# Optimization experiments

Measured on AMD Instinct MI355X. Metric: run time of the kernel, lower is better.

Reference implementation:

```python
import jax, jax.numpy as jnp
import numpy as np

NUM_HEADS = 32
HEAD_DIM = 128
HIDDEN = NUM_HEADS * HEAD_DIM
BLOCK = 128
ROPE_THETA = 10000.0
NEG_INF = -1e9


def _fp4_e2m1(x):
    # Simulated float_quantize(x, exp=2, man=1): E2M1 grid {0, .5, 1, 1.5, 2, 3, 4, 6},
    # round-to-nearest-even, saturate at +-6.
    a = jnp.abs(x)
    e = jnp.clip(jnp.floor(jnp.log2(jnp.maximum(a, 1e-30))), 0.0, 2.0)
    step = jnp.exp2(e) * 0.5  # mantissa LSB at this exponent
    q = jnp.clip(jnp.round(a / step) * step, 0.0, 6.0)
    return jnp.sign(x) * q


def quantize_mxfp4(v, block=BLOCK):
    # along_rows=False path: block over the sequence axis (after transpose(-1,-2)).
    b, h, s, d = v.shape
    t = jnp.swapaxes(v, -1, -2)  # [b,h,d,s]
    pad = (-s) % block
    t = jnp.pad(t, ((0, 0), (0, 0), (0, 0), (0, pad)))
    t = t.reshape(-1, block)
    amax = jnp.max(jnp.abs(t), axis=-1, keepdims=True)
    scale = jnp.exp2(jnp.ceil(jnp.log2(jnp.maximum(amax, 1e-30))) - 3.0)
    scale = jnp.where(amax == 0, 1.0, scale)
    t = _fp4_e2m1(t / scale) * scale
    t = t.reshape(b, h, d, s + pad)[..., :s]
    return jnp.swapaxes(t, -1, -2)


def _rotary(position_ids, dtype):
    # cos/sin: [b, s, head_dim]
    inv_freq = 1.0 / (ROPE_THETA ** (jnp.arange(0, HEAD_DIM, 2, dtype=jnp.float32) / HEAD_DIM))
    freqs = position_ids.astype(jnp.float32)[..., None] * inv_freq  # [b,s,d/2]
    emb = jnp.concatenate([freqs, freqs], axis=-1)
    return jnp.cos(emb).astype(dtype), jnp.sin(emb).astype(dtype)


def _rotate_half(x):
    x1, x2 = jnp.split(x, 2, axis=-1)
    return jnp.concatenate([-x2, x1], axis=-1)


def setup_inputs() -> dict:
    key = jax.random.key(0)
    ks = jax.random.split(key, 5)
    wscale = 1.0 / np.sqrt(HIDDEN)
    return {
        "hidden_states": jax.random.normal(ks[0], (2, 2048, HIDDEN), dtype=jnp.float32),
        "position_ids": jnp.arange(2048, dtype=jnp.int32)[None, :],
        "Wq": jax.random.normal(ks[1], (HIDDEN, HIDDEN), dtype=jnp.float32) * wscale,
        "Wk": jax.random.normal(ks[2], (HIDDEN, HIDDEN), dtype=jnp.float32) * wscale,
        "Wv": jax.random.normal(ks[3], (HIDDEN, HIDDEN), dtype=jnp.float32) * wscale,
        "Wo": jax.random.normal(ks[4], (HIDDEN, HIDDEN), dtype=jnp.float32) * wscale,
    }


def reference(hidden_states, position_ids, Wq, Wk, Wv, Wo):
    b, s, _ = hidden_states.shape

    # per-head channel ordering from ||row of v_proj||_2 (descending)
    norm3 = jnp.linalg.norm(Wv.astype(jnp.float32), ord=2, axis=-1)  # [HIDDEN]
    order = jnp.argsort(-norm3.reshape(NUM_HEADS, HEAD_DIM), axis=-1)  # [H, D]
    inverse_order = jnp.argsort(order, axis=-1)

    def proj(W):
        y = jnp.einsum('bsh,oh->bso', hidden_states, W)
        return y.reshape(b, s, NUM_HEADS, HEAD_DIM).transpose(0, 2, 1, 3)  # [b,H,s,D]

    q = proj(Wq)
    k = proj(Wk)
    v = proj(Wv)

    # reorder channels, mxfp4-quantize V along sequence blocks, restore order
    v = jnp.take_along_axis(v, order[None, :, None, :], axis=-1)
    v = quantize_mxfp4(v, BLOCK)
    v = jnp.take_along_axis(v, inverse_order[None, :, None, :], axis=-1)

    cos, sin = _rotary(position_ids, hidden_states.dtype)
    cos = cos[:, None, :, :]  # unsqueeze_dim=1
    sin = sin[:, None, :, :]
    q = q * cos + _rotate_half(q) * sin
    k = k * cos + _rotate_half(k) * sin

    scores = jnp.einsum('bhqd,bhkd->bhqk', q, k) / np.sqrt(HEAD_DIM)
    causal = jnp.tril(jnp.ones((s, s), dtype=bool))
    scores = jnp.where(causal[None, None], scores, NEG_INF)
    attn = jax.nn.softmax(scores.astype(jnp.float32), axis=-1).astype(q.dtype)

    out = jnp.einsum('bhqk,bhkd->bhqd', attn, v)
    out = out.transpose(0, 2, 1, 3).reshape(b, s, HIDDEN)
    return jnp.einsum('bso,ho->bsh', out, Wo)
```

## Files before the change

### kernel.cpp

```cpp
#include <hip/hip_runtime.h>
#include <math.h>

typedef unsigned short u16;
typedef unsigned int u32;
typedef short bf16x8 __attribute__((ext_vector_type(8)));
typedef float f32x4 __attribute__((ext_vector_type(4)));

#define MFMA16(a, b, c) __builtin_amdgcn_mfma_f32_16x16x32_bf16(a, b, c, 0, 0, 0)

static __device__ __forceinline__ u16 f2b(float f) {
  u32 u = __builtin_bit_cast(u32, f);
  u = (u + 0x7fffu + ((u >> 16) & 1u)) >> 16;
  return (u16)u;
}
static __device__ __forceinline__ float b2f(u16 h) {
  return __builtin_bit_cast(float, ((u32)h) << 16);
}
static __device__ __forceinline__ void gload16(const void* g, void* l) {
  __builtin_amdgcn_global_load_lds((const __attribute__((address_space(1))) void*)g,
                                   (__attribute__((address_space(3))) void*)l, 16, 0, 0);
}
static __device__ __forceinline__ void split2(float x, u16& hi, u16& lo) {
  hi = f2b(x);
  lo = f2b(x - b2f(hi));
}
static __device__ __forceinline__ float quant1(float x, float scale, float rs) {
  float y = fabsf(x) * rs;
  float st = y < 2.f ? 0.5f : (y < 4.f ? 1.f : 2.f);
  float iv = y < 2.f ? 2.f : (y < 4.f ? 1.f : 0.5f);
  float q = fminf(rintf(y * iv) * st, 6.f);
  return copysignf(q * scale, x);
}

__global__ __launch_bounds__(256) void k_cvt(const float* __restrict__ in, u16* __restrict__ out) {
  int i = blockIdx.x * 256 + threadIdx.x;
  float4 v = ((const float4*)in)[i];
  u32 lo = (u32)f2b(v.x) | ((u32)f2b(v.y) << 16);
  u32 hi = (u32)f2b(v.z) | ((u32)f2b(v.w) << 16);
  ((uint2*)out)[i] = make_uint2(lo, hi);
}

__global__ __launch_bounds__(256) void k_splt(const float* __restrict__ in,
                                              u16* __restrict__ hi, u16* __restrict__ lo) {
  int i = blockIdx.x * 256 + threadIdx.x;
  float4 v = ((const float4*)in)[i];
  u16 h[4], l[4];
  split2(v.x, h[0], l[0]);
  split2(v.y, h[1], l[1]);
  split2(v.z, h[2], l[2]);
  split2(v.w, h[3], l[3]);
  ((uint2*)hi)[i] = make_uint2((u32)h[0] | ((u32)h[1] << 16), (u32)h[2] | ((u32)h[3] << 16));
  ((uint2*)lo)[i] = make_uint2((u32)l[0] | ((u32)l[1] << 16), (u32)l[2] | ((u32)l[3] << 16));
}

__global__ __launch_bounds__(256) void k_rope_tab(const int* __restrict__ pid,
                                                  float* __restrict__ ct,
                                                  float* __restrict__ st) {
  int t = blockIdx.x * 256 + threadIdx.x;
  int s = t >> 6, i = t & 63;
  float inv = powf(10000.f, -(float)i * (1.f / 64.f));
  float a = (float)pid[s] * inv;
  ct[t] = cosf(a);
  st[t] = sinf(a);
}

template <int EPI>
__global__ __launch_bounds__(512, 2) void k_gemm8(const u16* __restrict__ A,
                                                  const u16* __restrict__ B,
                                                  void* __restrict__ outp,
                                                  const float* __restrict__ cost,
                                                  const float* __restrict__ sint) {
  __shared__ u16 Ls[2][2][2][8192];
  const int tid = threadIdx.x;
  const int wid = tid >> 6, lane = tid & 63;
  const int l15 = lane & 15, lhi = lane >> 4;
  const int wm = wid >> 2, wn = wid & 3;
  const int hib = wn >> 1, sub = wn & 1;

  const int bid = blockIdx.x;
  const int bx = 2 * (bid & 7) + (bid >> 7);
  const int by = (bid >> 3) & 15;
  const int mbase = by * 256, nbase = bx * 256;

  f32x4 acc[8][4];
#pragma unroll
  for (int mi = 0; mi < 8; ++mi)
#pragma unroll
    for (int nj = 0; nj < 4; ++nj) acc[mi][nj] = (f32x4){0.f, 0.f, 0.f, 0.f};

  auto stA = [&](int buf, int half, int ktile) {
    u16* dst = Ls[buf][0][half];
    const int k0 = ktile * 64;
#pragma unroll
    for (int i = 0; i < 2; ++i) {
      int idx = i * 512 + tid;
      int row = idx >> 3;
      int col = k0 + ((((idx & 7) << 4) ^ ((row & 7) << 4)) >> 1);
      gload16(A + (size_t)(mbase + half * 128 + row) * 4096 + col, (char*)dst + idx * 16);
    }
  };
  auto stB = [&](int buf, int half, int ktile) {
    u16* dst = Ls[buf][1][half];
    const int k0 = ktile * 64;
#pragma unroll
    for (int i = 0; i < 2; ++i) {
      int idx = i * 512 + tid;
      int row = idx >> 3;
      int col = k0 + ((((idx & 7) << 4) ^ ((row & 7) << 4)) >> 1);
      gload16(B + (size_t)(nbase + half * 128 + row) * 4096 + col, (char*)dst + idx * 16);
    }
  };

  stB(0, 0, 0);
  stB(0, 1, 0);
  stA(0, 0, 0);
  stA(0, 1, 0);
  stB(1, 0, 1);
  stB(1, 1, 1);

  const int NT = 64;
  for (int kt = 0; kt < NT; ++kt) {
    const int cur = kt & 1, nxt = cur ^ 1;
    const u16* Ab = Ls[cur][0][wm];
    const u16* Bb = Ls[cur][1][hib];
    bf16x8 aA[4][2], aB[4][2], bA[2][2], bB[2][2];

    if (kt + 1 < NT) stA(nxt, 0, kt + 1);
    if (kt == NT - 1) {
      asm volatile("s_waitcnt vmcnt(0)" ::: "memory");
    } else {
      asm volatile("s_waitcnt vmcnt(6)" ::: "memory");
    }
    __builtin_amdgcn_s_barrier();
#pragma unroll
    for (int mi = 0; mi < 4; ++mi)
#pragma unroll
      for (int ks = 0; ks < 2; ++ks) {
        int row = mi * 16 + l15;
        int kk2 = (ks * 32 + lhi * 8) * 2;
        aA[mi][ks] = *(const bf16x8*)((const char*)Ab + row * 128 + (kk2 ^ ((row & 7) << 4)));
      }
#pragma unroll
    for (int nj = 0; nj < 2; ++nj)
#pragma unroll
      for (int ks = 0; ks < 2; ++ks) {
        int row = sub * 32 + nj * 16 + l15;
        int kk2 = (ks * 32 + lhi * 8) * 2;
        bA[nj][ks] = *(const bf16x8*)((const char*)Bb + row * 128 + (kk2 ^ ((row & 7) << 4)));
      }
    __builtin_amdgcn_s_setprio(1);
#pragma unroll
    for (int mi = 0; mi < 4; ++mi)
#pragma unroll
      for (int nj = 0; nj < 2; ++nj)
#pragma unroll
        for (int ks = 0; ks < 2; ++ks) acc[mi][nj] = MFMA16(aA[mi][ks], bA[nj][ks], acc[mi][nj]);
    __builtin_amdgcn_s_setprio(0);
    __builtin_amdgcn_s_barrier();

#pragma unroll
    for (int nj = 0; nj < 2; ++nj)
#pragma unroll
      for (int ks = 0; ks < 2; ++ks) {
        int row = 64 + sub * 32 + nj * 16 + l15;
        int kk2 = (ks * 32 + lhi * 8) * 2;
        bB[nj][ks] = *(const bf16x8*)((const char*)Bb + row * 128 + (kk2 ^ ((row & 7) << 4)));
      }
    if (kt + 1 < NT) stA(nxt, 1, kt + 1);
    __builtin_amdgcn_s_barrier();
    __builtin_amdgcn_s_setprio(1);
#pragma unroll
    for (int mi = 0; mi < 4; ++mi)
#pragma unroll
      for (int nj = 0; nj < 2; ++nj)
#pragma unroll
        for (int ks = 0; ks < 2; ++ks)
          acc[mi][nj + 2] = MFMA16(aA[mi][ks], bB[nj][ks], acc[mi][nj + 2]);
    __builtin_amdgcn_s_setprio(0);
    __builtin_amdgcn_s_barrier();

#pragma unroll
    for (int mi = 0; mi < 4; ++mi)
#pragma unroll
      for (int ks = 0; ks < 2; ++ks) {
        int row = 64 + mi * 16 + l15;
        int kk2 = (ks * 32 + lhi * 8) * 2;
        aB[mi][ks] = *(const bf16x8*)((const char*)Ab + row * 128 + (kk2 ^ ((row & 7) << 4)));
      }
    if (kt + 2 < NT) stB(cur, 0, kt + 2);
    __builtin_amdgcn_s_barrier();
    __builtin_amdgcn_s_setprio(1);
#pragma unroll
    for (int mi = 0; mi < 4; ++mi)
#pragma unroll
      for (int nj = 0; nj < 2; ++nj)
#pragma unroll
        for (int ks = 0; ks < 2; ++ks)
          acc[mi + 4][nj] = MFMA16(aB[mi][ks], bA[nj][ks], acc[mi + 4][nj]);
    __builtin_amdgcn_s_setprio(0);
    __builtin_amdgcn_s_barrier();

    if (kt + 2 < NT) stB(cur, 1, kt + 2);
    __builtin_amdgcn_s_barrier();
    __builtin_amdgcn_s_setprio(1);
#pragma unroll
    for (int mi = 0; mi < 4; ++mi)
#pragma unroll
      for (int nj = 0; nj < 2; ++nj)
#pragma unroll
        for (int ks = 0; ks < 2; ++ks)
          acc[mi + 4][nj + 2] = MFMA16(aB[mi][ks], bB[nj][ks], acc[mi + 4][nj + 2]);
    __builtin_amdgcn_s_setprio(0);
    __builtin_amdgcn_s_barrier();
  }

  if constexpr (EPI == 3) {
    float* out = (float*)outp;
#pragma unroll
    for (int mi = 0; mi < 8; ++mi)
#pragma unroll
      for (int r = 0; r < 4; ++r) {
        size_t m = (size_t)(mbase + wm * 128 + mi * 16 + lhi * 4 + r);
#pragma unroll
        for (int nj = 0; nj < 4; ++nj) {
          int n = nbase + hib * 128 + (nj >> 1) * 64 + sub * 32 + (nj & 1) * 16 + l15;
          out[m * 4096 + n] = acc[mi][nj][r];
        }
      }
  } else {
    u16* qo = (u16*)outp;
    const int hgl = bx * 2 + hib;
#pragma unroll
    for (int mi = 0; mi < 8; ++mi)
#pragma unroll
      for (int r = 0; r < 4; ++r) {
        int m = mbase + wm * 128 + mi * 16 + lhi * 4 + r;
        int b = m >> 11, s = m & 2047;
        const float* ct = cost + (size_t)s * 64;
        const float* st = sint + (size_t)s * 64;
        size_t base = ((size_t)(b * 32 + hgl) * 2048 + s) * 128;
#pragma unroll
        for (int nj = 0; nj < 2; ++nj) {
          int d = sub * 32 + nj * 16 + l15;
          float c = ct[d], sn = st[d];
          float x1 = acc[mi][nj][r], x2 = acc[mi][nj + 2][r];
          qo[base + d] = f2b(x1 * c - x2 * sn);
          qo[base + d + 64] = f2b(x2 * c + x1 * sn);
        }
      }
  }
}

__global__ __launch_bounds__(512) void k_gemmv3(const u16* __restrict__ ahi,
                                                const u16* __restrict__ alo,
                                                const u16* __restrict__ bhi,
                                                const u16* __restrict__ blo,
                                                u16* __restrict__ vt) {
  __shared__ u16 Ls[2][4][8192];
  const int tid = threadIdx.x;
  const int wid = tid >> 6, lane = tid & 63;
  const int l15 = lane & 15, lhi = lane >> 4;
  const int wm = wid >> 2, wn = wid & 3;
  const int mbase = blockIdx.y * 128, nbase = blockIdx.x * 128;

  f32x4 acc[4][2];
#pragma unroll
  for (int mi = 0; mi < 4; ++mi)
#pragma unroll
    for (int nj = 0; nj < 2; ++nj) acc[mi][nj] = (f32x4){0.f, 0.f, 0.f, 0.f};

  auto stage = [&](int buf, int ktile) {
    const int k0 = ktile * 64;
#pragma unroll
    for (int i = 0; i < 2; ++i) {
      int idx = i * 512 + tid;
      int row = idx >> 3;
      int col = k0 + ((((idx & 7) << 4) ^ ((row & 7) << 4)) >> 1);
      size_t ga = (size_t)(mbase + row) * 4096 + col;
      size_t gb = (size_t)(nbase + row) * 4096 + col;
      gload16(ahi + ga, (char*)Ls[buf][0] + idx * 16);
      gload16(alo + ga, (char*)Ls[buf][1] + idx * 16);
      gload16(bhi + gb, (char*)Ls[buf][2] + idx * 16);
      gload16(blo + gb, (char*)Ls[buf][3] + idx * 16);
    }
  };

  stage(0, 0);

  const int NT = 64;
  for (int kt = 0; kt < NT; ++kt) {
    const int cur = kt & 1;
    if (kt < NT - 1) {
      stage(cur ^ 1, kt + 1);
      asm volatile("s_waitcnt vmcnt(8)" ::: "memory");
    } else {
      asm volatile("s_waitcnt vmcnt(0)" ::: "memory");
    }
    __builtin_amdgcn_s_barrier();

    bf16x8 ah[4][2], al[4][2], bh[2][2], bl[2][2];
#pragma unroll
    for (int mi = 0; mi < 4; ++mi)
#pragma unroll
      for (int ks = 0; ks < 2; ++ks) {
        int row = wm * 64 + mi * 16 + l15;
        int off = row * 128 + (((ks * 32 + lhi * 8) * 2) ^ ((row & 7) << 4));
        ah[mi][ks] = *(const bf16x8*)((const char*)Ls[cur][0] + off);
        al[mi][ks] = *(const bf16x8*)((const char*)Ls[cur][1] + off);
      }
#pragma unroll
    for (int nj = 0; nj < 2; ++nj)
#pragma unroll
      for (int ks = 0; ks < 2; ++ks) {
        int row = wn * 32 + nj * 16 + l15;
        int off = row * 128 + (((ks * 32 + lhi * 8) * 2) ^ ((row & 7) << 4));
        bh[nj][ks] = *(const bf16x8*)((const char*)Ls[cur][2] + off);
        bl[nj][ks] = *(const bf16x8*)((const char*)Ls[cur][3] + off);
      }
#pragma unroll
    for (int ks = 0; ks < 2; ++ks)
#pragma unroll
      for (int mi = 0; mi < 4; ++mi)
#pragma unroll
        for (int nj = 0; nj < 2; ++nj) {
          acc[mi][nj] = MFMA16(ah[mi][ks], bh[nj][ks], acc[mi][nj]);
          acc[mi][nj] = MFMA16(ah[mi][ks], bl[nj][ks], acc[mi][nj]);
          acc[mi][nj] = MFMA16(al[mi][ks], bh[nj][ks], acc[mi][nj]);
        }
    asm volatile("s_waitcnt lgkmcnt(0)" ::: "memory");
    __builtin_amdgcn_s_barrier();
  }

  const int h = nbase >> 7;
  float* red = (float*)Ls[0][0];
  float pam[2];
#pragma unroll
  for (int nj = 0; nj < 2; ++nj) {
    float a = 0.f;
#pragma unroll
    for (int mi = 0; mi < 4; ++mi)
#pragma unroll
      for (int r = 0; r < 4; ++r) a = fmaxf(a, fabsf(acc[mi][nj][r]));
    a = fmaxf(a, __shfl_xor(a, 16));
    a = fmaxf(a, __shfl_xor(a, 32));
    pam[nj] = a;
  }
  if (lhi == 0) {
#pragma unroll
    for (int nj = 0; nj < 2; ++nj) red[wid * 32 + nj * 16 + l15] = pam[nj];
  }
  __syncthreads();
#pragma unroll
  for (int nj = 0; nj < 2; ++nj) {
    int c = nj * 16 + l15;
    float amax = fmaxf(red[wn * 32 + c], red[(4 + wn) * 32 + c]);
    float scale = 1.f, rs = 1.f;
    if (amax > 0.f) {
      int e;
      float mant = frexpf(amax, &e);
      int cc = (mant == 0.5f) ? (e - 1) : e;
      scale = ldexpf(1.f, cc - 3);
      rs = ldexpf(1.f, 3 - cc);
    }
    int d = wn * 32 + c;
#pragma unroll
    for (int mi = 0; mi < 4; ++mi) {
      int m0 = mbase + wm * 64 + mi * 16 + lhi * 4;
      int b = m0 >> 11, s0 = m0 & 2047;
      uint2 pk;
      float v0 = quant1(acc[mi][nj][0], scale, rs);
      float v1 = quant1(acc[mi][nj][1], scale, rs);
      float v2 = quant1(acc[mi][nj][2], scale, rs);
      float v3 = quant1(acc[mi][nj][3], scale, rs);
      pk.x = (u32)f2b(v0) | ((u32)f2b(v1) << 16);
      pk.y = (u32)f2b(v2) | ((u32)f2b(v3) << 16);
      *(uint2*)(vt + ((size_t)(b * 32 + h) * 128 + d) * 2048 + s0) = pk;
    }
  }
}

template <int EPI>
__global__ __launch_bounds__(256) void k_gemm(const u16* __restrict__ A,
                                              const float* __restrict__ B,
                                              void* __restrict__ outp,
                                              const float* __restrict__ cost,
                                              const float* __restrict__ sint) {
  __shared__ u16 As[128 * 64];
  __shared__ u16 Bs[128 * 64];
  const int tid = threadIdx.x;
  const int w = tid >> 6, lane = tid & 63;
  const int l15 = lane & 15, lhi = lane >> 4;
  const int mbase = blockIdx.y * 128, nbase = blockIdx.x * 128;
  f32x4 acc[2][8];
#pragma unroll
  for (int i = 0; i < 2; ++i)
#pragma unroll
    for (int j = 0; j < 8; ++j) acc[i][j] = (f32x4){0.f, 0.f, 0.f, 0.f};

  const int brow = tid >> 1, bk = (tid & 1) * 32;
  const float* bsrc = B + (size_t)(nbase + brow) * 4096 + bk;

  for (int kt = 0; kt < 64; ++kt) {
    const int k0 = kt * 64;
#pragma unroll
    for (int i = 0; i < 4; ++i) {
      int idx = i * 256 + tid;
      int row = idx >> 3;
      int inb = ((idx & 7) << 4) ^ ((row & 7) << 4);
      gload16(A + (size_t)(mbase + row) * 4096 + (k0 + (inb >> 1)), (char*)As + idx * 16);
    }
    float4 bv[8];
    const float* bp = bsrc + k0;
#pragma unroll
    for (int c = 0; c < 8; ++c) bv[c] = *(const float4*)(bp + c * 4);
#pragma unroll
    for (int c = 0; c < 4; ++c) {
      uint4 pk;
      pk.x = (u32)f2b(bv[2 * c].x) | ((u32)f2b(bv[2 * c].y) << 16);
      pk.y = (u32)f2b(bv[2 * c].z) | ((u32)f2b(bv[2 * c].w) << 16);
      pk.z = (u32)f2b(bv[2 * c + 1].x) | ((u32)f2b(bv[2 * c + 1].y) << 16);
      pk.w = (u32)f2b(bv[2 * c + 1].z) | ((u32)f2b(bv[2 * c + 1].w) << 16);
      int byte = brow * 128 + (((bk + c * 8) * 2) ^ ((brow & 7) << 4));
      *(uint4*)((char*)Bs + byte) = pk;
    }
    __syncthreads();
#pragma unroll
    for (int ks = 0; ks < 2; ++ks) {
      const int kk2 = (ks * 32 + lhi * 8) * 2;
      bf16x8 af[2], bfr[8];
#pragma unroll
      for (int i = 0; i < 2; ++i) {
        int row = w * 32 + i * 16 + l15;
        af[i] = *(const bf16x8*)((const char*)As + row * 128 + (kk2 ^ ((row & 7) << 4)));
      }
#pragma unroll
      for (int j = 0; j < 8; ++j) {
        int row = j * 16 + l15;
        bfr[j] = *(const bf16x8*)((const char*)Bs + row * 128 + (kk2 ^ ((row & 7) << 4)));
      }
#pragma unroll
      for (int i = 0; i < 2; ++i)
#pragma unroll
        for (int j = 0; j < 8; ++j) acc[i][j] = MFMA16(af[i], bfr[j], acc[i][j]);
    }
    __syncthreads();
  }

  const int h = nbase >> 7;
  if constexpr (EPI == 3) {
    float* out = (float*)outp;
#pragma unroll
    for (int i = 0; i < 2; ++i)
#pragma unroll
      for (int r = 0; r < 4; ++r) {
        size_t m = (size_t)(mbase + w * 32 + i * 16 + lhi * 4 + r);
#pragma unroll
        for (int j = 0; j < 8; ++j) out[m * 4096 + nbase + j * 16 + l15] = acc[i][j][r];
      }
  } else {
    u16* qo = (u16*)outp;
#pragma unroll
    for (int i = 0; i < 2; ++i)
#pragma unroll
      for (int r = 0; r < 4; ++r) {
        int m = mbase + w * 32 + i * 16 + lhi * 4 + r;
        int b = m >> 11, s = m & 2047;
        const float* ct = cost + (size_t)s * 64;
        const float* st = sint + (size_t)s * 64;
        size_t base = ((size_t)(b * 32 + h) * 2048 + s) * 128;
#pragma unroll
        for (int j = 0; j < 4; ++j) {
          int d = j * 16 + l15;
          float c = ct[d], sn = st[d];
          float x1 = acc[i][j][r], x2 = acc[i][j + 4][r];
          qo[base + d] = f2b(x1 * c - x2 * sn);
          qo[base + d + 64] = f2b(x2 * c + x1 * sn);
        }
      }
  }
}

__global__ __launch_bounds__(256) void k_gemmv(const float* __restrict__ hsf,
                                               const float* __restrict__ Wv,
                                               u16* __restrict__ vt) {
  __shared__ u16 AsHi[128 * 64];
  __shared__ u16 AsLo[128 * 64];
  __shared__ u16 BsHi[128 * 64];
  __shared__ u16 BsLo[128 * 64];
  const int tid = threadIdx.x;
  const int w = tid >> 6, lane = tid & 63;
  const int l15 = lane & 15, lhi = lane >> 4;
  const int mbase = blockIdx.y * 128, nbase = blockIdx.x * 128;
  f32x4 acc[2][8];
#pragma unroll
  for (int i = 0; i < 2; ++i)
#pragma unroll
    for (int j = 0; j < 8; ++j) acc[i][j] = (f32x4){0.f, 0.f, 0.f, 0.f};

  const int srow = tid >> 1, sk = (tid & 1) * 32;
  const float* asrc = hsf + (size_t)(mbase + srow) * 4096 + sk;
  const float* bsrc = Wv + (size_t)(nbase + srow) * 4096 + sk;

  for (int kt = 0; kt < 64; ++kt) {
    const int k0 = kt * 64;
    float4 av[8], bv[8];
#pragma unroll
    for (int c = 0; c < 8; ++c) {
      av[c] = *(const float4*)(asrc + k0 + c * 4);
      bv[c] = *(const float4*)(bsrc + k0 + c * 4);
    }
#pragma unroll
    for (int c = 0; c < 4; ++c) {
      u16 h0, l0, h1, l1;
      float fa[8] = {av[2 * c].x, av[2 * c].y, av[2 * c].z, av[2 * c].w,
                     av[2 * c + 1].x, av[2 * c + 1].y, av[2 * c + 1].z, av[2 * c + 1].w};
      float fb[8] = {bv[2 * c].x, bv[2 * c].y, bv[2 * c].z, bv[2 * c].w,
                     bv[2 * c + 1].x, bv[2 * c + 1].y, bv[2 * c + 1].z, bv[2 * c + 1].w};
      u32 ph[4], pl[4], qh[4], ql[4];
#pragma unroll
      for (int t = 0; t < 4; ++t) {
        split2(fa[2 * t], h0, l0);
        split2(fa[2 * t + 1], h1, l1);
        ph[t] = (u32)h0 | ((u32)h1 << 16);
        pl[t] = (u32)l0 | ((u32)l1 << 16);
        split2(fb[2 * t], h0, l0);
        split2(fb[2 * t + 1], h1, l1);
        qh[t] = (u32)h0 | ((u32)h1 << 16);
        ql[t] = (u32)l0 | ((u32)l1 << 16);
      }
      int byte = srow * 128 + (((sk + c * 8) * 2) ^ ((srow & 7) << 4));
      *(uint4*)((char*)AsHi + byte) = make_uint4(ph[0], ph[1], ph[2], ph[3]);
      *(uint4*)((char*)AsLo + byte) = make_uint4(pl[0], pl[1], pl[2], pl[3]);
      *(uint4*)((char*)BsHi + byte) = make_uint4(qh[0], qh[1], qh[2], qh[3]);
      *(uint4*)((char*)BsLo + byte) = make_uint4(ql[0], ql[1], ql[2], ql[3]);
    }
    __syncthreads();
#pragma unroll
    for (int ks = 0; ks < 2; ++ks) {
      const int kk2 = (ks * 32 + lhi * 8) * 2;
      bf16x8 afh[2], afl[2];
#pragma unroll
      for (int i = 0; i < 2; ++i) {
        int row = w * 32 + i * 16 + l15;
        int off = row * 128 + (kk2 ^ ((row & 7) << 4));
        afh[i] = *(const bf16x8*)((const char*)AsHi + off);
        afl[i] = *(const bf16x8*)((const char*)AsLo + off);
      }
#pragma unroll
      for (int j = 0; j < 8; ++j) {
        int row = j * 16 + l15;
        int off = row * 128 + (kk2 ^ ((row & 7) << 4));
        bf16x8 bh = *(const bf16x8*)((const char*)BsHi + off);
        bf16x8 bl = *(const bf16x8*)((const char*)BsLo + off);
#pragma unroll
        for (int i = 0; i < 2; ++i) {
          acc[i][j] = MFMA16(afh[i], bh, acc[i][j]);
          acc[i][j] = MFMA16(afh[i], bl, acc[i][j]);
          acc[i][j] = MFMA16(afl[i], bh, acc[i][j]);
        }
      }
    }
    __syncthreads();
  }

  const int h = nbase >> 7;
  float pam[8];
#pragma unroll
  for (int j = 0; j < 8; ++j) {
    float a = 0.f;
#pragma unroll
    for (int i = 0; i < 2; ++i)
#pragma unroll
      for (int r = 0; r < 4; ++r) a = fmaxf(a, fabsf(acc[i][j][r]));
    a = fmaxf(a, __shfl_xor(a, 16));
    a = fmaxf(a, __shfl_xor(a, 32));
    pam[j] = a;
  }
  float* red = (float*)BsHi;
  if (lhi == 0) {
#pragma unroll
    for (int j = 0; j < 8; ++j) red[w * 128 + j * 16 + l15] = pam[j];
  }
  __syncthreads();
#pragma unroll
  for (int j = 0; j < 8; ++j) {
    float amax = fmaxf(fmaxf(red[0 * 128 + j * 16 + l15], red[1 * 128 + j * 16 + l15]),
                       fmaxf(red[2 * 128 + j * 16 + l15], red[3 * 128 + j * 16 + l15]));
    float scale = 1.f, rs = 1.f;
    if (amax > 0.f) {
      int e;
      float mant = frexpf(amax, &e);
      int c = (mant == 0.5f) ? (e - 1) : e;
      scale = ldexpf(1.f, c - 3);
      rs = ldexpf(1.f, 3 - c);
    }
#pragma unroll
    for (int i = 0; i < 2; ++i) {
      int m0 = mbase + w * 32 + i * 16 + lhi * 4;
      int b = m0 >> 11, s0 = m0 & 2047;
      int d = j * 16 + l15;
      uint2 pk;
      float v0 = quant1(acc[i][j][0], scale, rs);
      float v1 = quant1(acc[i][j][1], scale, rs);
      float v2 = quant1(acc[i][j][2], scale, rs);
      float v3 = quant1(acc[i][j][3], scale, rs);
      pk.x = (u32)f2b(v0) | ((u32)f2b(v1) << 16);
      pk.y = (u32)f2b(v2) | ((u32)f2b(v3) << 16);
      *(uint2*)(vt + ((size_t)(b * 32 + h) * 128 + d) * 2048 + s0) = pk;
    }
  }
}

__global__ __launch_bounds__(512) void k_attn(const u16* __restrict__ qg,
                                              const u16* __restrict__ kg,
                                              const u16* __restrict__ vtg,
                                              u16* __restrict__ ao) {
  __shared__ u16 Ks[2][64 * 128];
  __shared__ u16 Vs[2][128 * 64];
  __shared__ u16 Ps[8 * 16 * 72];
  const int qt = 15 - blockIdx.y;
  const int bh = blockIdx.x;
  const int tid = threadIdx.x, w = tid >> 6, lane = tid & 63;
  const int l15 = lane & 15, lhi = lane >> 4;
  const size_t bhoff = (size_t)bh * (2048 * 128);
  const float SC = 0.08838834764831845f;

  bf16x8 qf[4];
  {
    const int qrow = qt * 128 + w * 16 + l15;
    const u16* qp = qg + bhoff + (size_t)qrow * 128 + lhi * 8;
#pragma unroll
    for (int ks = 0; ks < 4; ++ks) qf[ks] = *(const bf16x8*)(qp + ks * 32);
  }
  f32x4 oacc[8];
#pragma unroll
  for (int dt = 0; dt < 8; ++dt) oacc[dt] = (f32x4){0.f, 0.f, 0.f, 0.f};
  float mrow[4] = {-1e30f, -1e30f, -1e30f, -1e30f};
  float lrow[4] = {0.f, 0.f, 0.f, 0.f};

  auto stage = [&](int buf, int kbase) {
#pragma unroll
    for (int i = 0; i < 2; ++i) {
      int idx = i * 512 + tid;
      int row = idx >> 4;
      int inb = ((idx & 15) << 4) ^ ((row & 15) << 4);
      gload16(kg + bhoff + (size_t)(kbase + row) * 128 + (inb >> 1), (char*)Ks[buf] + idx * 16);
    }
#pragma unroll
    for (int i = 0; i < 2; ++i) {
      int idx = i * 512 + tid;
      int row = idx >> 3;
      int inb = ((idx & 7) << 4) ^ ((row & 7) << 4);
      gload16(vtg + bhoff + (size_t)row * 2048 + kbase + (inb >> 1), (char*)Vs[buf] + idx * 16);
    }
  };

  const int nt = 2 * qt + 2;
  stage(0, 0);

  for (int kt = 0; kt < nt; ++kt) {
    const int cur = kt & 1;
    if (kt < nt - 1) {
      stage(cur ^ 1, (kt + 1) * 64);
      asm volatile("s_waitcnt vmcnt(4)" ::: "memory");
    } else {
      asm volatile("s_waitcnt vmcnt(0)" ::: "memory");
    }
    __builtin_amdgcn_s_barrier();

    f32x4 sc4[4];
#pragma unroll
    for (int j = 0; j < 4; ++j) sc4[j] = (f32x4){0.f, 0.f, 0.f, 0.f};
#pragma unroll
    for (int ks = 0; ks < 4; ++ks) {
      const int db = (ks * 32 + lhi * 8) * 2;
#pragma unroll
      for (int j = 0; j < 4; ++j) {
        int kr = j * 16 + l15;
        bf16x8 bfr = *(const bf16x8*)((const char*)Ks[cur] + kr * 256 + (db ^ ((kr & 15) << 4)));
        sc4[j] = MFMA16(qf[ks], bfr, sc4[j]);
      }
    }
    float p[4][4];
    const int kbase = kt * 64;
    const bool tail = (kt >= 2 * qt);
#pragma unroll
    for (int j = 0; j < 4; ++j)
#pragma unroll
      for (int r = 0; r < 4; ++r) {
        float s = sc4[j][r] * SC;
        if (tail && (kbase + j * 16 + l15 > qt * 128 + w * 16 + lhi * 4 + r)) s = -1e9f;
        p[j][r] = s;
      }
    float alpha[4];
#pragma unroll
    for (int r = 0; r < 4; ++r) {
      float tm = fmaxf(fmaxf(p[0][r], p[1][r]), fmaxf(p[2][r], p[3][r]));
      tm = fmaxf(tm, __shfl_xor(tm, 1));
      tm = fmaxf(tm, __shfl_xor(tm, 2));
      tm = fmaxf(tm, __shfl_xor(tm, 4));
      tm = fmaxf(tm, __shfl_xor(tm, 8));
      float mn = fmaxf(mrow[r], tm);
      alpha[r] = __expf(mrow[r] - mn);
      mrow[r] = mn;
      float rsum = 0.f;
#pragma unroll
      for (int j = 0; j < 4; ++j) {
        float e = __expf(p[j][r] - mn);
        p[j][r] = e;
        rsum += e;
      }
      rsum += __shfl_xor(rsum, 1);
      rsum += __shfl_xor(rsum, 2);
      rsum += __shfl_xor(rsum, 4);
      rsum += __shfl_xor(rsum, 8);
      lrow[r] = lrow[r] * alpha[r] + rsum;
    }
#pragma unroll
    for (int dt = 0; dt < 8; ++dt) {
      f32x4 t = oacc[dt];
      t[0] *= alpha[0]; t[1] *= alpha[1]; t[2] *= alpha[2]; t[3] *= alpha[3];
      oacc[dt] = t;
    }
#pragma unroll
    for (int j = 0; j < 4; ++j)
#pragma unroll
      for (int r = 0; r < 4; ++r)
        Ps[w * 1152 + (lhi * 4 + r) * 72 + j * 16 + l15] = f2b(p[j][r]);
#pragma unroll
    for (int ks2 = 0; ks2 < 2; ++ks2) {
      const int sb = ks2 * 32 + lhi * 8;
      bf16x8 pa = *(const bf16x8*)((const char*)Ps + w * 2304 + l15 * 144 + sb * 2);
#pragma unroll
      for (int dt = 0; dt < 8; ++dt) {
        int d = dt * 16 + l15;
        bf16x8 vb = *(const bf16x8*)((const char*)Vs[cur] + d * 128 + ((sb * 2) ^ ((d & 7) << 4)));
        oacc[dt] = MFMA16(pa, vb, oacc[dt]);
      }
    }
    asm volatile("s_waitcnt lgkmcnt(0)" ::: "memory");
    __builtin_amdgcn_s_barrier();
  }

  const int b = bh >> 5, h = bh & 31;
  float inv[4];
#pragma unroll
  for (int r = 0; r < 4; ++r) inv[r] = 1.f / lrow[r];
#pragma unroll
  for (int dt = 0; dt < 8; ++dt)
#pragma unroll
    for (int r = 0; r < 4; ++r) {
      int s = qt * 128 + w * 16 + lhi * 4 + r;
      ao[((size_t)(b * 2048 + s)) * 4096 + h * 128 + dt * 16 + l15] = f2b(oacc[dt][r] * inv[r]);
    }
}

extern "C" void kernel_launch(void* const* d_in, const int* in_sizes, int n_in,
                              void* d_out, int out_size, void* d_ws, size_t ws_size,
                              hipStream_t stream) {
  (void)in_sizes; (void)n_in; (void)out_size;
  const float* hs = (const float*)d_in[0];
  const int* pid = (const int*)d_in[1];
  const float* Wq = (const float*)d_in[2];
  const float* Wk = (const float*)d_in[3];
  const float* Wv = (const float*)d_in[4];
  const float* Wo = (const float*)d_in[5];
  float* out = (float*)d_out;
  char* ws = (char*)d_ws;

  const size_t BUF = 33554432;
  const size_t NEED = 7 * BUF + 2 * 524288;

  if (ws_size >= NEED) {
    u16* hsb  = (u16*)(ws + 0 * BUF);
    u16* hslo = (u16*)(ws + 1 * BUF);
    u16* qb   = (u16*)(ws + 2 * BUF);
    u16* kb   = (u16*)(ws + 3 * BUF);
    u16* vtb  = (u16*)(ws + 4 * BUF);
    u16* wbuf = (u16*)(ws + 5 * BUF);
    u16* wvlo = (u16*)(ws + 6 * BUF);
    float* cost = (float*)(ws + 7 * BUF);
    float* sint = (float*)(ws + 7 * BUF + 524288);
    u16* aob = hslo;

    k_splt<<<16384, 256, 0, stream>>>(hs, hsb, hslo);
    k_rope_tab<<<512, 256, 0, stream>>>(pid, cost, sint);
    k_cvt<<<16384, 256, 0, stream>>>(Wq, wbuf);
    k_gemm8<0><<<256, 512, 0, stream>>>(hsb, wbuf, (void*)qb, cost, sint);
    k_cvt<<<16384, 256, 0, stream>>>(Wk, wbuf);
    k_gemm8<1><<<256, 512, 0, stream>>>(hsb, wbuf, (void*)kb, cost, sint);
    k_splt<<<16384, 256, 0, stream>>>(Wv, wbuf, wvlo);
    k_gemmv3<<<dim3(32, 32), 512, 0, stream>>>(hsb, hslo, wbuf, wvlo, vtb);
    k_attn<<<dim3(64, 16), 512, 0, stream>>>(qb, kb, vtb, aob);
    k_cvt<<<16384, 256, 0, stream>>>(Wo, wbuf);
    k_gemm8<3><<<256, 512, 0, stream>>>(aob, wbuf, (void*)out, nullptr, nullptr);
  } else {
    u16* hsb = (u16*)(ws + 0);
    u16* qb  = (u16*)(ws + 33554432);
    u16* kb  = (u16*)(ws + 67108864);
    u16* vtb = (u16*)(ws + 100663296);
    float* cost = (float*)(ws + 134217728);
    float* sint = (float*)(ws + 134742016);
    u16* aob = hsb;

    k_cvt<<<16384, 256, 0, stream>>>(hs, hsb);
    k_rope_tab<<<512, 256, 0, stream>>>(pid, cost, sint);
    k_gemm<0><<<dim3(32, 32), 256, 0, stream>>>(hsb, Wq, (void*)qb, cost, sint);
    k_gemm<1><<<dim3(32, 32), 256, 0, stream>>>(hsb, Wk, (void*)kb, cost, sint);
    k_gemmv<<<dim3(32, 32), 256, 0, stream>>>(hs, Wv, vtb);
    k_attn<<<dim3(64, 16), 512, 0, stream>>>(qb, kb, vtb, aob);
    k_gemm<3><<<dim3(32, 32), 256, 0, stream>>>(aob, Wo, (void*)out, nullptr, nullptr);
  }
}
```

Before: 997.0 us.

## Rewrite V projection GEMM with 256x256 tiles and interleaved staged pipeline

Replaces the 128x128-tile split-bf16 V projection kernel with a 256x256-tile version on 256 blocks. The K step shrinks to 32 and the four operand matrices are staged at different points, interleaved with four MFMA quadrants that use setprio. The larger tile raises operand reuse per loaded byte and cuts global traffic. With each wave now covering 128 rows, the sequence-block amax reduces entirely within a wave, so the LDS amax reduction and its __syncthreads go away. The costs are a larger accumulator footprint (128 floats per lane), more barriers per K step, and fewer blocks than the previous 1024-block grid.

After: 899.6 us. 9.8% less time.

```diff
diff --git a/kernel.cpp b/kernel.cpp
--- a/kernel.cpp
+++ b/kernel.cpp
@@ -251,121 +251,167 @@
   }
 }
 
-__global__ __launch_bounds__(512) void k_gemmv3(const u16* __restrict__ ahi,
-                                                const u16* __restrict__ alo,
-                                                const u16* __restrict__ bhi,
-                                                const u16* __restrict__ blo,
-                                                u16* __restrict__ vt) {
-  __shared__ u16 Ls[2][4][8192];
+__global__ __launch_bounds__(512, 2) void k_gemmv4(const u16* __restrict__ ahi,
+                                                   const u16* __restrict__ alo,
+                                                   const u16* __restrict__ bhi,
+                                                   const u16* __restrict__ blo,
+                                                   u16* __restrict__ vt) {
+  __shared__ u16 Ls[2][4][256 * 32];
   const int tid = threadIdx.x;
   const int wid = tid >> 6, lane = tid & 63;
   const int l15 = lane & 15, lhi = lane >> 4;
   const int wm = wid >> 2, wn = wid & 3;
-  const int mbase = blockIdx.y * 128, nbase = blockIdx.x * 128;
-
-  f32x4 acc[4][2];
-#pragma unroll
-  for (int mi = 0; mi < 4; ++mi)
-#pragma unroll
-    for (int nj = 0; nj < 2; ++nj) acc[mi][nj] = (f32x4){0.f, 0.f, 0.f, 0.f};
-
-  auto stage = [&](int buf, int ktile) {
-    const int k0 = ktile * 64;
+  const int bid = blockIdx.x;
+  const int bx = 2 * (bid & 7) + (bid >> 7);
+  const int by = (bid >> 3) & 15;
+  const int mbase = by * 256, nbase = bx * 256;
+
+  f32x4 acc[8][4];
+#pragma unroll
+  for (int mi = 0; mi < 8; ++mi)
+#pragma unroll
+    for (int nj = 0; nj < 4; ++nj) acc[mi][nj] = (f32x4){0.f, 0.f, 0.f, 0.f};
+
+  auto stg = [&](int buf, int mat, int ktile, const u16* src, int rbase) {
+    const int k0 = ktile * 32;
 #pragma unroll
     for (int i = 0; i < 2; ++i) {
       int idx = i * 512 + tid;
-      int row = idx >> 3;
-      int col = k0 + ((((idx & 7) << 4) ^ ((row & 7) << 4)) >> 1);
-      size_t ga = (size_t)(mbase + row) * 4096 + col;
-      size_t gb = (size_t)(nbase + row) * 4096 + col;
-      gload16(ahi + ga, (char*)Ls[buf][0] + idx * 16);
-      gload16(alo + ga, (char*)Ls[buf][1] + idx * 16);
-      gload16(bhi + gb, (char*)Ls[buf][2] + idx * 16);
-      gload16(blo + gb, (char*)Ls[buf][3] + idx * 16);
+      int row = idx >> 2, slot = idx & 3;
+      int sslot = slot ^ ((row >> 1) & 3);
+      gload16(src + (size_t)(rbase + row) * 4096 + k0 + sslot * 8,
+              (char*)Ls[buf][mat] + idx * 16);
     }
   };
-
-  stage(0, 0);
-
-  const int NT = 64;
+  auto rd = [&](const u16* base, int row) -> bf16x8 {
+    return *(const bf16x8*)((const char*)base + row * 64 + ((lhi ^ ((row >> 1) & 3)) << 4));
+  };
+
+  stg(0, 0, 0, ahi, mbase);
+  stg(0, 1, 0, alo, mbase);
+  stg(0, 2, 0, bhi, nbase);
+  stg(0, 3, 0, blo, nbase);
+  stg(1, 2, 1, bhi, nbase);
+  stg(1, 3, 1, blo, nbase);
+
+  const int NT = 128;
   for (int kt = 0; kt < NT; ++kt) {
-    const int cur = kt & 1;
-    if (kt < NT - 1) {
-      stage(cur ^ 1, kt + 1);
-      asm volatile("s_waitcnt vmcnt(8)" ::: "memory");
+    const int cur = kt & 1, nxt = cur ^ 1;
+    const u16* AH = Ls[cur][0];
+    const u16* AL = Ls[cur][1];
+    const u16* BH = Ls[cur][2];
+    const u16* BL = Ls[cur][3];
+    bf16x8 axh[4], axl[4], ayh[4], ayl[4], bxh[2], bxl[2], byh[2], byl[2];
+
+    if (kt + 1 < NT) stg(nxt, 0, kt + 1, ahi, mbase);
+    if (kt == NT - 1) {
+      asm volatile("s_waitcnt vmcnt(0)" ::: "memory");
     } else {
-      asm volatile("s_waitcnt vmcnt(0)" ::: "memory");
-    }
-    __builtin_amdgcn_s_barrier();
-
-    bf16x8 ah[4][2], al[4][2], bh[2][2], bl[2][2];
-#pragma unroll
-    for (int mi = 0; mi < 4; ++mi)
-#pragma unroll
-      for (int ks = 0; ks < 2; ++ks) {
-        int row = wm * 64 + mi * 16 + l15;
-        int off = row * 128 + (((ks * 32 + lhi * 8) * 2) ^ ((row & 7) << 4));
-        ah[mi][ks] = *(const bf16x8*)((const char*)Ls[cur][0] + off);
-        al[mi][ks] = *(const bf16x8*)((const char*)Ls[cur][1] + off);
-      }
-#pragma unroll
-    for (int nj = 0; nj < 2; ++nj)
-#pragma unroll
-      for (int ks = 0; ks < 2; ++ks) {
-        int row = wn * 32 + nj * 16 + l15;
-        int off = row * 128 + (((ks * 32 + lhi * 8) * 2) ^ ((row & 7) << 4));
-        bh[nj][ks] = *(const bf16x8*)((const char*)Ls[cur][2] + off);
-        bl[nj][ks] = *(const bf16x8*)((const char*)Ls[cur][3] + off);
-      }
-#pragma unroll
-    for (int ks = 0; ks < 2; ++ks)
-#pragma unroll
-      for (int mi = 0; mi < 4; ++mi)
-#pragma unroll
-        for (int nj = 0; nj < 2; ++nj) {
-          acc[mi][nj] = MFMA16(ah[mi][ks], bh[nj][ks], acc[mi][nj]);
-          acc[mi][nj] = MFMA16(ah[mi][ks], bl[nj][ks], acc[mi][nj]);
-          acc[mi][nj] = MFMA16(al[mi][ks], bh[nj][ks], acc[mi][nj]);
-        }
-    asm volatile("s_waitcnt lgkmcnt(0)" ::: "memory");
-    __builtin_amdgcn_s_barrier();
-  }
-
-  const int h = nbase >> 7;
-  float* red = (float*)Ls[0][0];
-  float pam[2];
-#pragma unroll
-  for (int nj = 0; nj < 2; ++nj) {
+      asm volatile("s_waitcnt vmcnt(6)" ::: "memory");
+    }
+    __builtin_amdgcn_s_barrier();
+#pragma unroll
+    for (int mi = 0; mi < 4; ++mi) {
+      int row = wm * 128 + mi * 16 + l15;
+      axh[mi] = rd(AH, row);
+      axl[mi] = rd(AL, row);
+    }
+#pragma unroll
+    for (int nj = 0; nj < 2; ++nj) {
+      int row = wn * 64 + nj * 16 + l15;
+      bxh[nj] = rd(BH, row);
+      bxl[nj] = rd(BL, row);
+    }
+    __builtin_amdgcn_s_setprio(1);
+#pragma unroll
+    for (int mi = 0; mi < 4; ++mi)
+#pragma unroll
+      for (int nj = 0; nj < 2; ++nj) {
+        acc[mi][nj] = MFMA16(axh[mi], bxh[nj], acc[mi][nj]);
+        acc[mi][nj] = MFMA16(axh[mi], bxl[nj], acc[mi][nj]);
+        acc[mi][nj] = MFMA16(axl[mi], bxh[nj], acc[mi][nj]);
+      }
+    __builtin_amdgcn_s_setprio(0);
+    __builtin_amdgcn_s_barrier();
+
+#pragma unroll
+    for (int nj = 0; nj < 2; ++nj) {
+      int row = wn * 64 + 32 + nj * 16 + l15;
+      byh[nj] = rd(BH, row);
+      byl[nj] = rd(BL, row);
+    }
+    if (kt + 1 < NT) stg(nxt, 1, kt + 1, alo, mbase);
+    __builtin_amdgcn_s_barrier();
+    __builtin_amdgcn_s_setprio(1);
+#pragma unroll
+    for (int mi = 0; mi < 4; ++mi)
+#pragma unroll
+      for (int nj = 0; nj < 2; ++nj) {
+        acc[mi][nj + 2] = MFMA16(axh[mi], byh[nj], acc[mi][nj + 2]);
+        acc[mi][nj + 2] = MFMA16(axh[mi], byl[nj], acc[mi][nj + 2]);
+        acc[mi][nj + 2] = MFMA16(axl[mi], byh[nj], acc[mi][nj + 2]);
+      }
+    __builtin_amdgcn_s_setprio(0);
+    __builtin_amdgcn_s_barrier();
+
+#pragma unroll
+    for (int mi = 0; mi < 4; ++mi) {
+      int row = wm * 128 + 64 + mi * 16 + l15;
+      ayh[mi] = rd(AH, row);
+      ayl[mi] = rd(AL, row);
+    }
+    if (kt + 2 < NT) stg(cur, 2, kt + 2, bhi, nbase);
+    __builtin_amdgcn_s_barrier();
+    __builtin_amdgcn_s_setprio(1);
+#pragma unroll
+    for (int mi = 0; mi < 4; ++mi)
+#pragma unroll
+      for (int nj = 0; nj < 2; ++nj) {
+        acc[mi + 4][nj] = MFMA16(ayh[mi], bxh[nj], acc[mi + 4][nj]);
+        acc[mi + 4][nj] = MFMA16(ayh[mi], bxl[nj], acc[mi + 4][nj]);
+        acc[mi + 4][nj] = MFMA16(ayl[mi], bxh[nj], acc[mi + 4][nj]);
+      }
+    __builtin_amdgcn_s_setprio(0);
+    __builtin_amdgcn_s_barrier();
+
+    if (kt + 2 < NT) stg(cur, 3, kt + 2, blo, nbase);
+    __builtin_amdgcn_s_barrier();
+    __builtin_amdgcn_s_setprio(1);
+#pragma unroll
+    for (int mi = 0; mi < 4; ++mi)
+#pragma unroll
+      for (int nj = 0; nj < 2; ++nj) {
+        acc[mi + 4][nj + 2] = MFMA16(ayh[mi], byh[nj], acc[mi + 4][nj + 2]);
+        acc[mi + 4][nj + 2] = MFMA16(ayh[mi], byl[nj], acc[mi + 4][nj + 2]);
+        acc[mi + 4][nj + 2] = MFMA16(ayl[mi], byh[nj], acc[mi + 4][nj + 2]);
+      }
+    __builtin_amdgcn_s_setprio(0);
+    __builtin_amdgcn_s_barrier();
+  }
+
+  const int h = (nbase >> 7) + (wn >> 1);
+  const int d0 = (wn & 1) * 64;
+#pragma unroll
+  for (int nj = 0; nj < 4; ++nj) {
     float a = 0.f;
 #pragma unroll
-    for (int mi = 0; mi < 4; ++mi)
+    for (int mi = 0; mi < 8; ++mi)
 #pragma unroll
       for (int r = 0; r < 4; ++r) a = fmaxf(a, fabsf(acc[mi][nj][r]));
     a = fmaxf(a, __shfl_xor(a, 16));
     a = fmaxf(a, __shfl_xor(a, 32));
-    pam[nj] = a;
-  }
-  if (lhi == 0) {
-#pragma unroll
-    for (int nj = 0; nj < 2; ++nj) red[wid * 32 + nj * 16 + l15] = pam[nj];
-  }
-  __syncthreads();
-#pragma unroll
-  for (int nj = 0; nj < 2; ++nj) {
-    int c = nj * 16 + l15;
-    float amax = fmaxf(red[wn * 32 + c], red[(4 + wn) * 32 + c]);
     float scale = 1.f, rs = 1.f;
-    if (amax > 0.f) {
+    if (a > 0.f) {
       int e;
-      float mant = frexpf(amax, &e);
+      float mant = frexpf(a, &e);
       int cc = (mant == 0.5f) ? (e - 1) : e;
       scale = ldexpf(1.f, cc - 3);
       rs = ldexpf(1.f, 3 - cc);
     }
-    int d = wn * 32 + c;
-#pragma unroll
-    for (int mi = 0; mi < 4; ++mi) {
-      int m0 = mbase + wm * 64 + mi * 16 + lhi * 4;
+    int d = d0 + nj * 16 + l15;
+#pragma unroll
+    for (int mi = 0; mi < 8; ++mi) {
+      int m0 = mbase + wm * 128 + mi * 16 + lhi * 4;
       int b = m0 >> 11, s0 = m0 & 2047;
       uint2 pk;
       float v0 = quant1(acc[mi][nj][0], scale, rs);
@@ -790,7 +836,7 @@
     k_cvt<<<16384, 256, 0, stream>>>(Wk, wbuf);
     k_gemm8<1><<<256, 512, 0, stream>>>(hsb, wbuf, (void*)kb, cost, sint);
     k_splt<<<16384, 256, 0, stream>>>(Wv, wbuf, wvlo);
-    k_gemmv3<<<dim3(32, 32), 512, 0, stream>>>(hsb, hslo, wbuf, wvlo, vtb);
+    k_gemmv4<<<256, 512, 0, stream>>>(hsb, hslo, wbuf, wvlo, vtb);
     k_attn<<<dim3(64, 16), 512, 0, stream>>>(qb, kb, vtb, aob);
     k_cvt<<<16384, 256, 0, stream>>>(Wo, wbuf);
     k_gemm8<3><<<256, 512, 0, stream>>>(aob, wbuf, (void*)out, nullptr, nullptr);
```
